# Kernel optimization log

Hardware: AMD Instinct MI355X
Metric: run time of the kernel (lower is better)

## Reference

```python
import jax, jax.numpy as jnp
import numpy as np

B, S, D, H, NL = 4, 1024, 512, 8, 2
DFF = 4 * D
EPS = 1e-5


def _layernorm(x, g, b):
    m = x.mean(-1, keepdims=True)
    v = ((x - m) ** 2).mean(-1, keepdims=True)
    return (x - m) / jnp.sqrt(v + EPS) * g + b


def _forward(x, Wq, bq, Wk, bk, Wv, bv, Wo, bo, W1, b1, W2, b2, ln1_g, ln1_b, ln2_g, ln2_b):
    Bn, Sn, Dn = x.shape
    Nl, Hh = Wq.shape[0], Wq.shape[1]
    dk = Dn // Hh  # scaling uses dmodel//h even though heads are full-width (faithful to SDPA)
    for i in range(Nl):
        # per-head full-width projections: each head maps dmodel -> dmodel
        q = jnp.einsum('bsd,hed->bhse', x, Wq[i]) + bq[i][:, None, :]
        k = jnp.einsum('bsd,hed->bhse', x, Wk[i]) + bk[i][:, None, :]
        v = jnp.einsum('bsd,hed->bhse', x, Wv[i]) + bv[i][:, None, :]
        scores = jnp.einsum('bhse,bhte->bhst', q, k) / jnp.sqrt(jnp.asarray(dk, x.dtype))
        attn = jax.nn.softmax(scores, axis=-1)
        heads = jnp.einsum('bhst,bhte->bhse', attn, v)          # [B,H,S,D]
        cat = heads.transpose(0, 2, 1, 3).reshape(Bn, Sn, Hh * Dn)  # concat heads -> [B,S,H*D]
        mha_out = cat @ Wo[i].T + bo[i]
        x = _layernorm(x + mha_out, ln1_g[i], ln1_b[i])
        ff = jax.nn.relu(x @ W1[i].T + b1[i]) @ W2[i].T + b2[i]
        x = _layernorm(x + ff, ln2_g[i], ln2_b[i])
    return x


def setup_inputs() -> dict:
    key = jax.random.key(0)
    ks = jax.random.split(key, 12)
    def w(k, shape, fan_in):
        return (jax.random.normal(k, shape, jnp.float32) / np.sqrt(fan_in)).astype(jnp.float32)
    inp = {
        'x': jax.random.normal(ks[0], (B, S, D), jnp.float32),
        'Wq': w(ks[1], (NL, H, D, D), D), 'bq': jnp.zeros((NL, H, D), jnp.float32),
        'Wk': w(ks[2], (NL, H, D, D), D), 'bk': jnp.zeros((NL, H, D), jnp.float32),
        'Wv': w(ks[3], (NL, H, D, D), D), 'bv': jnp.zeros((NL, H, D), jnp.float32),
        'Wo': w(ks[4], (NL, D, H * D), H * D), 'bo': jnp.zeros((NL, D), jnp.float32),
        'W1': w(ks[5], (NL, DFF, D), D), 'b1': jnp.zeros((NL, DFF), jnp.float32),
        'W2': w(ks[6], (NL, D, DFF), DFF), 'b2': jnp.zeros((NL, D), jnp.float32),
        'ln1_g': jnp.ones((NL, D), jnp.float32), 'ln1_b': jnp.zeros((NL, D), jnp.float32),
        'ln2_g': jnp.ones((NL, D), jnp.float32), 'ln2_b': jnp.zeros((NL, D), jnp.float32),
    }
    return inp


def reference(x, Wq, bq, Wk, bk, Wv, bv, Wo, bo, W1, b1, W2, b2, ln1_g, ln1_b, ln2_g, ln2_b):
    return _forward(x, Wq, bq, Wk, bk, Wv, bv, Wo, bo, W1, b1, W2, b2, ln1_g, ln1_b, ln2_g, ln2_b)
```

## Files before the change

### kernel.cpp

```cpp
#include <hip/hip_runtime.h>
#include <cstdint>
#include <cstddef>

#define NB 4
#define NS 1024
#define ND 512
#define NH 8
#define NLAYER 2
#define NDFF 2048

typedef __attribute__((ext_vector_type(8))) short short8;
typedef __attribute__((ext_vector_type(4))) float f32x4;
typedef __attribute__((ext_vector_type(4))) unsigned short u16x4;
typedef unsigned short u16;
typedef long long ll;

__device__ __forceinline__ float b2f(u16 u) {
  union { unsigned int i; float f; } x; x.i = ((unsigned int)u) << 16; return x.f;
}
__device__ __forceinline__ u16 f2b(float f) {
  union { float f; unsigned int i; } x; x.f = f;
  return (u16)((x.i + 0x7FFF + ((x.i >> 16) & 1)) >> 16);
}

struct Zm { int div; ll hi, lo; };
__device__ __forceinline__ ll zoff(Zm m, int z) {
  return (ll)(z / m.div) * m.hi + (ll)(z % m.div) * m.lo;
}

enum { F_BF16 = 1, F_RELU = 2, F_BCOL = 4, F_BROW = 8, F_RESID = 16 };

__device__ __forceinline__ void load_lds16(const void* g, void* s) {
  __builtin_amdgcn_global_load_lds(
      (const __attribute__((address_space(1))) void*)(uintptr_t)g,
      (__attribute__((address_space(3))) void*)(uint32_t)(uintptr_t)s, 16, 0, 0);
}

#define MFMA16(d, a, b) \
  asm volatile("v_mfma_f32_16x16x32_bf16 %0, %1, %2, %0" : "+v"(d) : "v"(a), "v"(b))

__global__ void __launch_bounds__(256)
gemm_bt(const u16* __restrict__ A, int lda, Zm za,
        const u16* __restrict__ Bw, int ldb, Zm zb,
        const u16* __restrict__ Bw2, const float* __restrict__ bias2, int zsplit,
        void* __restrict__ Cv, int ldc, Zm zc,
        const float* __restrict__ bias, Zm zbias,
        const float* __restrict__ resid,
        float scale, int K, int flags)
{
  __shared__ __align__(16) char smem[2][16384];

  const int gx = gridDim.x, gy = gridDim.y;
  int id = (blockIdx.z * gy + blockIdx.y) * gx + blockIdx.x;
  const int nwg = gx * gy * (int)gridDim.z;
  if ((nwg & 7) == 0) id = (id & 7) * (nwg >> 3) + (id >> 3);
  const int bx = id % gx;
  const int rest = id / gx;
  const int by = rest % gy;
  const int z0 = rest / gy;

  int zB = z0;
  const u16* Bsel = Bw;
  const float* bsel = bias;
  if (z0 >= zsplit) { Bsel = Bw2; bsel = bias2; zB = z0 - zsplit; }

  A    += zoff(za, z0);
  Bsel += zoff(zb, zB);

  const int bm = by * 128, bn = bx * 128;
  const int t = threadIdx.x;
  const int w = t >> 6, lane = t & 63;
  const int wr = w >> 1, wc = w & 1;

  const u16* ga0 = A    + (size_t)(bm + (t >> 2)) * lda + ((t & 3) << 3);
  const u16* ga1 = ga0 + (size_t)64 * lda;
  const u16* gb0 = Bsel + (size_t)(bn + (t >> 2)) * ldb + ((t & 3) << 3);
  const u16* gb1 = gb0 + (size_t)64 * ldb;

  auto STAGE = [&](int sel, int kt) {
    const int k0 = kt << 5;
    char* sa = smem[sel] + (w << 10);
    char* sb = smem[sel] + 8192 + (w << 10);
    load_lds16(ga0 + k0, sa);
    load_lds16(ga1 + k0, sa + 4096);
    load_lds16(gb0 + k0, sb);
    load_lds16(gb1 + k0, sb + 4096);
  };

  f32x4 acc[4][4];
#pragma unroll
  for (int i = 0; i < 4; ++i)
#pragma unroll
    for (int j = 0; j < 4; ++j) acc[i][j] = (f32x4){0.f, 0.f, 0.f, 0.f};

  const int fr = lane & 15;
  const int kg = (lane >> 4) << 3;

  const int nt = K >> 5;
  STAGE(0, 0);
  __syncthreads();
  int cur = 0;
  for (int kt = 0; kt < nt; ++kt) {
    if (kt + 1 < nt) STAGE(cur ^ 1, kt + 1);
    const u16* la = (const u16*)smem[cur];
    const u16* lb = (const u16*)(smem[cur] + 8192);
    short8 af[4], bf[4];
#pragma unroll
    for (int mi = 0; mi < 4; ++mi)
      af[mi] = *(const short8*)(la + (wr * 64 + mi * 16 + fr) * 32 + kg);
#pragma unroll
    for (int ni = 0; ni < 4; ++ni)
      bf[ni] = *(const short8*)(lb + (wc * 64 + ni * 16 + fr) * 32 + kg);
#pragma unroll
    for (int mi = 0; mi < 4; ++mi)
#pragma unroll
      for (int ni = 0; ni < 4; ++ni)
        MFMA16(acc[mi][ni], af[mi], bf[ni]);
    __syncthreads();
    cur ^= 1;
  }

  asm volatile("s_nop 7\n\ts_nop 7" ::: "memory");

  const ll co = zoff(zc, z0);
  const float* bz = (flags & (F_BCOL | F_BROW)) ? bsel + zoff(zbias, zB) : nullptr;
  const int r0 = (lane >> 4) << 2;
  const int c0 = lane & 15;
#pragma unroll
  for (int mi = 0; mi < 4; ++mi) {
#pragma unroll
    for (int ni = 0; ni < 4; ++ni) {
#pragma unroll
      for (int r = 0; r < 4; ++r) {
        const int grow = bm + wr * 64 + mi * 16 + r0 + r;
        const int gcol = bn + wc * 64 + ni * 16 + c0;
        float v = acc[mi][ni][r] * scale;
        if (flags & F_BCOL) v += bz[gcol];
        if (flags & F_BROW) v += bz[grow];
        if (flags & F_RELU) v = fmaxf(v, 0.f);
        if (flags & F_RESID) v += resid[(size_t)grow * ldc + gcol];
        const ll idx = co + (ll)grow * ldc + gcol;
        if (flags & F_BF16) ((u16*)Cv)[idx] = f2b(v);
        else                ((float*)Cv)[idx] = v;
      }
    }
  }
}

__global__ void __launch_bounds__(256)
fattn(const u16* __restrict__ qg, const u16* __restrict__ kg,
      const u16* __restrict__ vtg, u16* __restrict__ cat)
{
  __shared__ __align__(16) u16 stg[2][64 * 128];
  __shared__ __align__(16) u16 p_lds[64 * 64];

  int id = blockIdx.x;
  id = (id & 7) * 64 + (id >> 3);
  const int qt = id & 15;
  const int hb = id >> 4;
  const int h = hb >> 2, b = hb & 3;

  const ll hbase = (ll)h * NB * NS * ND;
  const u16* Q  = qg  + hbase + (ll)(b * NS + qt * 64) * ND;
  const u16* Kp = kg  + hbase + (ll)b * NS * ND;
  const u16* VT = vtg + (ll)hb * ND * NS;
  u16* Op = cat + (ll)(b * NS + qt * 64) * (NH * ND) + h * ND;

  const int t = threadIdx.x;
  const int w = t >> 6, lane = t & 63;
  const int fr = lane & 15, khi = lane >> 4;

  short8 qreg[16];
#pragma unroll
  for (int s = 0; s < 16; ++s)
    qreg[s] = *(const short8*)(Q + (ll)(w * 16 + fr) * ND + s * 32 + khi * 8);

  const int srowK = t >> 4;
  const int scolK = (((t & 15) ^ (srowK & 7)) << 3);
  const int srowV = t >> 3;
  const int scolV = (((t & 7) ^ (srowV & 7)) << 3);
  const int wofs = w << 10;

  auto STG_K = [&](int buf, int kv, int dch) {
#pragma unroll
    for (int i = 0; i < 4; ++i)
      load_lds16(Kp + (ll)(kv * 64 + i * 16 + srowK) * ND + dch * 128 + scolK,
                 (char*)stg[buf] + i * 4096 + wofs);
  };
  auto STG_V = [&](int buf, int kv, int ec) {
#pragma unroll
    for (int i = 0; i < 4; ++i)
      load_lds16(VT + (ll)(ec * 128 + i * 32 + srowV) * NS + kv * 64 + scolV,
                 (char*)stg[buf] + i * 4096 + wofs);
  };

  f32x4 o[4][8];
#pragma unroll
  for (int ec = 0; ec < 4; ++ec)
#pragma unroll
    for (int nf = 0; nf < 8; ++nf) o[ec][nf] = (f32x4){0.f, 0.f, 0.f, 0.f};
  float m_r[4] = {-1e30f, -1e30f, -1e30f, -1e30f};
  float l_r[4] = {0.f, 0.f, 0.f, 0.f};

  STG_K(0, 0, 0);
  __syncthreads();
  int cur = 0;

  for (int kv = 0; kv < 16; ++kv) {
    f32x4 s[4];
#pragma unroll
    for (int nf = 0; nf < 4; ++nf) s[nf] = (f32x4){0.f, 0.f, 0.f, 0.f};

#pragma unroll
    for (int dch = 0; dch < 4; ++dch) {
      if (dch < 3) STG_K(cur ^ 1, kv, dch + 1);
      else         STG_V(cur ^ 1, kv, 0);
      const u16* kb_ = stg[cur];
#pragma unroll
      for (int ks = 0; ks < 4; ++ks) {
        const short8 aq = qreg[dch * 4 + ks];
#pragma unroll
        for (int nf = 0; nf < 4; ++nf) {
          const short8 bk = *(const short8*)(
              kb_ + (nf * 16 + fr) * 128 + ((((4 * ks + khi)) ^ (fr & 7)) << 3));
          MFMA16(s[nf], aq, bk);
        }
      }
      __syncthreads();
      cur ^= 1;
    }
    asm volatile("s_nop 7\n\ts_nop 7" ::: "memory");

    float mxs[4];
    bool big = false;
#pragma unroll
    for (int r = 0; r < 4; ++r) {
      float mx = s[0][r];
#pragma unroll
      for (int nf = 1; nf < 4; ++nf) mx = fmaxf(mx, s[nf][r]);
      mx *= 0.125f;
      mx = fmaxf(mx, __shfl_xor(mx, 1));
      mx = fmaxf(mx, __shfl_xor(mx, 2));
      mx = fmaxf(mx, __shfl_xor(mx, 4));
      mx = fmaxf(mx, __shfl_xor(mx, 8));
      mxs[r] = mx;
      big = big || (mx > m_r[r] + 8.f);
    }
    const bool resc = __any(big);
    float f_r[4];
#pragma unroll
    for (int r = 0; r < 4; ++r) {
      const float mn = resc ? fmaxf(m_r[r], mxs[r]) : m_r[r];
      f_r[r] = resc ? __expf(m_r[r] - mn) : 1.f;
      m_r[r] = mn;
      float sum = 0.f;
      const int R = w * 16 + 4 * khi + r;
#pragma unroll
      for (int nf = 0; nf < 4; ++nf) {
        const float e = __expf(s[nf][r] * 0.125f - mn);
        sum += e;
        const int g = (nf * 2 + (fr >> 3)) ^ ((4 * khi + r) & 7);
        p_lds[R * 64 + (g << 3) + (fr & 7)] = f2b(e);
      }
      sum += __shfl_xor(sum, 1);
      sum += __shfl_xor(sum, 2);
      sum += __shfl_xor(sum, 4);
      sum += __shfl_xor(sum, 8);
      l_r[r] = l_r[r] * f_r[r] + sum;
    }
    if (resc) {
#pragma unroll
      for (int ec = 0; ec < 4; ++ec)
#pragma unroll
        for (int nf = 0; nf < 8; ++nf)
#pragma unroll
          for (int r = 0; r < 4; ++r) o[ec][nf][r] *= f_r[r];
    }

    short8 ap[2];
#pragma unroll
    for (int ks2 = 0; ks2 < 2; ++ks2)
      ap[ks2] = *(const short8*)(
          p_lds + (w * 16 + fr) * 64 + ((((4 * ks2 + khi)) ^ (fr & 7)) << 3));

#pragma unroll
    for (int ec = 0; ec < 4; ++ec) {
      if (ec < 3)           STG_V(cur ^ 1, kv, ec + 1);
      else if (kv < 15)     STG_K(cur ^ 1, kv + 1, 0);
      const u16* vb = stg[cur];
#pragma unroll
      for (int ks2 = 0; ks2 < 2; ++ks2)
#pragma unroll
        for (int nf = 0; nf < 8; ++nf) {
          const short8 bv = *(const short8*)(
              vb + (nf * 16 + fr) * 64 + ((((4 * ks2 + khi)) ^ (fr & 7)) << 3));
          MFMA16(o[ec][nf], ap[ks2], bv);
        }
      __syncthreads();
      cur ^= 1;
    }
  }

  asm volatile("s_nop 7\n\ts_nop 7" ::: "memory");
#pragma unroll
  for (int r = 0; r < 4; ++r) {
    const float inv = 1.f / l_r[r];
    const ll row = (ll)(w * 16 + 4 * khi + r) * (NH * ND);
#pragma unroll
    for (int ec = 0; ec < 4; ++ec)
#pragma unroll
      for (int nf = 0; nf < 8; ++nf)
        Op[row + ec * 128 + nf * 16 + fr] = f2b(o[ec][nf][r] * inv);
  }
}

__global__ void __launch_bounds__(256)
ln_red(const float* __restrict__ parts, int np, ll pstride,
       const float* __restrict__ bias, const float* __restrict__ resid,
       const float* __restrict__ g, const float* __restrict__ be,
       float* __restrict__ xout, u16* __restrict__ xbout)
{
  const int t = threadIdx.x, w = t >> 6, lane = t & 63;
  const ll row = (ll)blockIdx.x * 4 + w;
  const ll base = row * ND + lane * 8;
  float v[8];
  *(f32x4*)(v)     = *(const f32x4*)(resid + base);
  *(f32x4*)(v + 4) = *(const f32x4*)(resid + base + 4);
#pragma unroll
  for (int j = 0; j < 8; ++j) v[j] += bias[lane * 8 + j];
  for (int pIdx = 0; pIdx < np; ++pIdx) {
    const float* pp = parts + pIdx * pstride + base;
    f32x4 a0 = *(const f32x4*)(pp);
    f32x4 a1 = *(const f32x4*)(pp + 4);
    v[0] += a0.x; v[1] += a0.y; v[2] += a0.z; v[3] += a0.w;
    v[4] += a1.x; v[5] += a1.y; v[6] += a1.z; v[7] += a1.w;
  }
  float s = 0.f, q = 0.f;
#pragma unroll
  for (int j = 0; j < 8; ++j) { s += v[j]; q += v[j] * v[j]; }
#pragma unroll
  for (int o = 32; o >= 1; o >>= 1) { s += __shfl_xor(s, o); q += __shfl_xor(q, o); }
  const float mean = s * (1.f / ND);
  const float var  = q * (1.f / ND) - mean * mean;
  const float inv  = 1.f / sqrtf(var + 1e-5f);
#pragma unroll
  for (int j = 0; j < 8; ++j) {
    const int c = lane * 8 + j;
    const float y = (v[j] - mean) * inv * g[c] + be[c];
    xout[row * ND + c] = y;
    xbout[row * ND + c] = f2b(y);
  }
}

struct CvtJobs { const float* src[7]; u16* dst[7]; ll n[7]; };

__global__ void __launch_bounds__(256)
cvt7(CvtJobs j)
{
  const int z = blockIdx.y;
  const ll i = ((ll)blockIdx.x * 256 + threadIdx.x) * 4;
  if (i >= j.n[z]) return;
  f32x4 v = *(const f32x4*)(j.src[z] + i);
  u16x4 o;
  o.x = f2b(v.x); o.y = f2b(v.y); o.z = f2b(v.z); o.w = f2b(v.w);
  *(u16x4*)(j.dst[z] + i) = o;
}

extern "C" void kernel_launch(void* const* d_in, const int* in_sizes, int n_in,
                              void* d_out, int out_size, void* d_ws, size_t ws_size,
                              hipStream_t stream)
{
  (void)in_sizes; (void)n_in; (void)out_size; (void)ws_size;
  const float* x_in = (const float*)d_in[0];
  const float* Wq = (const float*)d_in[1];  const float* bq = (const float*)d_in[2];
  const float* Wk = (const float*)d_in[3];  const float* bk = (const float*)d_in[4];
  const float* Wv = (const float*)d_in[5];  const float* bv = (const float*)d_in[6];
  const float* Wo = (const float*)d_in[7];  const float* bo = (const float*)d_in[8];
  const float* W1 = (const float*)d_in[9];  const float* b1 = (const float*)d_in[10];
  const float* W2 = (const float*)d_in[11]; const float* b2 = (const float*)d_in[12];
  const float* ln1g = (const float*)d_in[13]; const float* ln1b = (const float*)d_in[14];
  const float* ln2g = (const float*)d_in[15]; const float* ln2b = (const float*)d_in[16];

  char* p = (char*)d_ws;
  auto alloc = [&](ll bytes) { char* r = p; p += (bytes + 255) & ~(ll)255; return r; };
  const ll nWq = (ll)NLAYER * NH * ND * ND;
  const ll nWo = (ll)NLAYER * ND * NH * ND;
  const ll nW1 = (ll)NLAYER * NDFF * ND;
  const ll nX  = (ll)NB * NS * ND;

  u16* wq_b = (u16*)alloc(nWq * 2);
  u16* wk_b = (u16*)alloc(nWq * 2);
  u16* wv_b = (u16*)alloc(nWq * 2);
  u16* wo_b = (u16*)alloc(nWo * 2);
  u16* w1_b = (u16*)alloc(nW1 * 2);
  u16* w2_b = (u16*)alloc(nW1 * 2);
  u16* xb   = (u16*)alloc(nX * 2);
  u16* qb   = (u16*)alloc((ll)NH * NB * NS * ND * 2);
  u16* kb   = (u16*)alloc((ll)NH * NB * NS * ND * 2);
  u16* vT   = (u16*)alloc((ll)NH * NB * ND * NS * 2);
  u16* scb  = (u16*)alloc((ll)NB * NH * NS * NS * 2);
  u16* cat = scb;
  float* parts = (float*)(scb + (ll)NB * NS * NH * ND);
  u16* ffh = qb;

  CvtJobs cj;
  cj.src[0] = Wq; cj.dst[0] = wq_b; cj.n[0] = nWq;
  cj.src[1] = Wk; cj.dst[1] = wk_b; cj.n[1] = nWq;
  cj.src[2] = Wv; cj.dst[2] = wv_b; cj.n[2] = nWq;
  cj.src[3] = Wo; cj.dst[3] = wo_b; cj.n[3] = nWo;
  cj.src[4] = W1; cj.dst[4] = w1_b; cj.n[4] = nW1;
  cj.src[5] = W2; cj.dst[5] = w2_b; cj.n[5] = nW1;
  cj.src[6] = x_in; cj.dst[6] = xb; cj.n[6] = nX;
  cvt7<<<dim3((unsigned)((nWq / 4 + 255) / 256), 7), 256, 0, stream>>>(cj);

  float* xf = (float*)d_out;
  const Zm Z0{1, 0, 0};
  const ll PSTR = nX;
  const int ZINF = 1 << 30;

  for (int i = 0; i < NLAYER; ++i) {
    const float* resid1 = (i == 0) ? x_in : xf;
    const ll woff = (ll)i * NH * ND * ND;

    gemm_bt<<<dim3(ND/128, (NB*NS)/128, 2*NH), 256, 0, stream>>>(
        xb, ND, Z0,
        wq_b + woff, ND, Zm{1, (ll)ND * ND, 0},
        wk_b + woff, bk + (ll)i * NH * ND, NH,
        qb, ND, Zm{1, (ll)NB * NS * ND, 0},
        bq + (ll)i * NH * ND, Zm{1, ND, 0}, nullptr, 1.f, ND, F_BF16 | F_BCOL);

    gemm_bt<<<dim3(NS/128, ND/128, NH*NB), 256, 0, stream>>>(
        wv_b + woff, ND, Zm{NB, (ll)ND * ND, 0},
        xb, ND, Zm{NB, 0, (ll)NS * ND},
        xb, nullptr, ZINF,
        vT, NS, Zm{1, (ll)ND * NS, 0},
        bv + (ll)i * NH * ND, Zm{NB, ND, 0}, nullptr, 1.f, ND, F_BF16 | F_BROW);

    fattn<<<dim3(512), 256, 0, stream>>>(qb, kb, vT, cat);

    gemm_bt<<<dim3(ND/128, (NB*NS)/128, 4), 256, 0, stream>>>(
        cat, NH * ND, Zm{1, 1024, 0},
        wo_b + (ll)i * ND * NH * ND, NH * ND, Zm{1, 1024, 0},
        wo_b, nullptr, ZINF,
        parts, ND, Zm{1, PSTR, 0},
        nullptr, Z0, nullptr, 1.f, 1024, 0);

    ln_red<<<dim3(NB * NS / 4), 256, 0, stream>>>(
        parts, 4, PSTR, bo + (ll)i * ND, resid1,
        ln1g + (ll)i * ND, ln1b + (ll)i * ND, xf, xb);

    gemm_bt<<<dim3(NDFF/128, (NB*NS)/128, 1), 256, 0, stream>>>(
        xb, ND, Z0,
        w1_b + (ll)i * NDFF * ND, ND, Z0,
        w1_b, nullptr, ZINF,
        ffh, NDFF, Z0,
        b1 + (ll)i * NDFF, Z0, nullptr, 1.f, ND, F_BF16 | F_BCOL | F_RELU);

    gemm_bt<<<dim3(ND/128, (NB*NS)/128, 4), 256, 0, stream>>>(
        ffh, NDFF, Zm{1, 512, 0},
        w2_b + (ll)i * ND * NDFF, NDFF, Zm{1, 512, 0},
        w2_b, nullptr, ZINF,
        parts, ND, Zm{1, PSTR, 0},
        nullptr, Z0, nullptr, 1.f, 512, 0);

    ln_red<<<dim3(NB * NS / 4), 256, 0, stream>>>(
        parts, 4, PSTR, b2 + (ll)i * ND, xf,
        ln2g + (ll)i * ND, ln2b + (ll)i * ND, xf, xb);
  }
}
```

Baseline: 783.1 us.

## Triple-buffer attention K/V staging with prefetch distance two and vmcnt waits

The flash-attention kernel moves from a double-buffered LDS staging scheme with a full __syncthreads per phase to a three-buffer ring. Each K or V chunk is prefetched two phases ahead, and the wait uses s_waitcnt vmcnt plus a bare s_barrier, so loads overlap more MFMA work. The P tile also switches from an XOR swizzle to a padded 72-element row stride. The change costs more shared memory, which may lower occupancy, and depends on the exact vmcnt counts being correct for each stage.

```diff
diff --git a/kernel.cpp b/kernel.cpp
--- a/kernel.cpp
+++ b/kernel.cpp
@@ -38,6 +38,8 @@
 
 #define MFMA16(d, a, b) \
   asm volatile("v_mfma_f32_16x16x32_bf16 %0, %1, %2, %0" : "+v"(d) : "v"(a), "v"(b))
+#define WAITVM(n) asm volatile("s_waitcnt vmcnt(" #n ")" ::: "memory")
+#define BAR() __builtin_amdgcn_s_barrier()
 
 __global__ void __launch_bounds__(256)
 gemm_bt(const u16* __restrict__ A, int lda, Zm za,
@@ -151,8 +153,8 @@
 fattn(const u16* __restrict__ qg, const u16* __restrict__ kg,
       const u16* __restrict__ vtg, u16* __restrict__ cat)
 {
-  __shared__ __align__(16) u16 stg[2][64 * 128];
-  __shared__ __align__(16) u16 p_lds[64 * 64];
+  __shared__ __align__(16) u16 stg[3][64 * 128];
+  __shared__ __align__(16) u16 p_lds[64 * 72];
 
   int id = blockIdx.x;
   id = (id & 7) * 64 + (id >> 3);
@@ -193,6 +195,12 @@
       load_lds16(VT + (ll)(ec * 128 + i * 32 + srowV) * NS + kv * 64 + scolV,
                  (char*)stg[buf] + i * 4096 + wofs);
   };
+  auto STAGE_PH = [&](int g) {
+    const int kvv = g >> 3, pp = g & 7;
+    if (kvv >= 16) return;
+    if (pp < 4) STG_K(g % 3, kvv, pp);
+    else        STG_V(g % 3, kvv, pp - 4);
+  };
 
   f32x4 o[4][8];
 #pragma unroll
@@ -202,9 +210,8 @@
   float m_r[4] = {-1e30f, -1e30f, -1e30f, -1e30f};
   float l_r[4] = {0.f, 0.f, 0.f, 0.f};
 
-  STG_K(0, 0, 0);
-  __syncthreads();
-  int cur = 0;
+  STAGE_PH(0);
+  STAGE_PH(1);
 
   for (int kv = 0; kv < 16; ++kv) {
     f32x4 s[4];
@@ -212,22 +219,21 @@
     for (int nf = 0; nf < 4; ++nf) s[nf] = (f32x4){0.f, 0.f, 0.f, 0.f};
 
 #pragma unroll
-    for (int dch = 0; dch < 4; ++dch) {
-      if (dch < 3) STG_K(cur ^ 1, kv, dch + 1);
-      else         STG_V(cur ^ 1, kv, 0);
-      const u16* kb_ = stg[cur];
+    for (int p = 0; p < 4; ++p) {
+      WAITVM(4);
+      BAR();
+      STAGE_PH(kv * 8 + p + 2);
+      const u16* kb_ = stg[(kv * 8 + p) % 3];
 #pragma unroll
       for (int ks = 0; ks < 4; ++ks) {
-        const short8 aq = qreg[dch * 4 + ks];
+        const short8 aq = qreg[p * 4 + ks];
 #pragma unroll
         for (int nf = 0; nf < 4; ++nf) {
           const short8 bk = *(const short8*)(
-              kb_ + (nf * 16 + fr) * 128 + ((((4 * ks + khi)) ^ (fr & 7)) << 3));
+              kb_ + (nf * 16 + fr) * 128 + (((4 * ks + khi) ^ (fr & 7)) << 3));
           MFMA16(s[nf], aq, bk);
         }
       }
-      __syncthreads();
-      cur ^= 1;
     }
     asm volatile("s_nop 7\n\ts_nop 7" ::: "memory");
 
@@ -259,8 +265,7 @@
       for (int nf = 0; nf < 4; ++nf) {
         const float e = __expf(s[nf][r] * 0.125f - mn);
         sum += e;
-        const int g = (nf * 2 + (fr >> 3)) ^ ((4 * khi + r) & 7);
-        p_lds[R * 64 + (g << 3) + (fr & 7)] = f2b(e);
+        p_lds[R * 72 + nf * 16 + fr] = f2b(e);
       }
       sum += __shfl_xor(sum, 1);
       sum += __shfl_xor(sum, 2);
@@ -277,27 +282,27 @@
           for (int r = 0; r < 4; ++r) o[ec][nf][r] *= f_r[r];
     }
 
+    asm volatile("s_waitcnt lgkmcnt(0)" ::: "memory");
+    __builtin_amdgcn_sched_barrier(0);
     short8 ap[2];
 #pragma unroll
     for (int ks2 = 0; ks2 < 2; ++ks2)
-      ap[ks2] = *(const short8*)(
-          p_lds + (w * 16 + fr) * 64 + ((((4 * ks2 + khi)) ^ (fr & 7)) << 3));
-
-#pragma unroll
-    for (int ec = 0; ec < 4; ++ec) {
-      if (ec < 3)           STG_V(cur ^ 1, kv, ec + 1);
-      else if (kv < 15)     STG_K(cur ^ 1, kv + 1, 0);
-      const u16* vb = stg[cur];
+      ap[ks2] = *(const short8*)(p_lds + (w * 16 + fr) * 72 + 32 * ks2 + 8 * khi);
+
+#pragma unroll
+    for (int p2 = 0; p2 < 4; ++p2) {
+      if (kv == 15 && p2 == 3) { WAITVM(0); } else { WAITVM(4); }
+      BAR();
+      STAGE_PH(kv * 8 + 4 + p2 + 2);
+      const u16* vb = stg[(kv * 8 + 4 + p2) % 3];
 #pragma unroll
       for (int ks2 = 0; ks2 < 2; ++ks2)
 #pragma unroll
         for (int nf = 0; nf < 8; ++nf) {
           const short8 bv = *(const short8*)(
-              vb + (nf * 16 + fr) * 64 + ((((4 * ks2 + khi)) ^ (fr & 7)) << 3));
-          MFMA16(o[ec][nf], ap[ks2], bv);
+              vb + (nf * 16 + fr) * 64 + (((4 * ks2 + khi) ^ (fr & 7)) << 3));
+          MFMA16(o[p2][nf], ap[ks2], bv);
         }
-      __syncthreads();
-      cur ^= 1;
     }
   }
 
```

Measured after the change: 794.6 us. About the same (+1.5%).
